# Kernel tuning notes

Measured on AMD Instinct MI355X. Metric: run time of the kernel, lower is better.

## Reference

```python
import jax, jax.numpy as jnp
import numpy as np

K = 4      # tagset_size - 2 (real emotion tags)
NT = 6     # tagset_size
START = 4
STOP = 5


def setup_inputs() -> dict:
    key = jax.random.key(0)
    ks = jax.random.split(key, 10)
    B, T = 2048, 2048
    feats = jax.random.normal(ks[0], (B, T, NT), dtype=jnp.float32)
    bias = jax.random.uniform(ks[1], (B, T), dtype=jnp.float32)        # bias_dict values in [0,1)
    tags = jax.random.randint(ks[2], (B, T), 0, K)                     # emotion labels only
    transitions = jax.random.normal(ks[3], (NT, NT), dtype=jnp.float32)
    transitions = transitions.at[START, :].set(-10000.0)
    transitions = transitions.at[:, STOP].set(-10000.0)
    w_shift_in = jax.random.normal(ks[4], (K,), dtype=jnp.float32)
    bias_no = jax.random.normal(ks[5], (1,), dtype=jnp.float32)
    bias_with = jax.random.normal(ks[6], (1,), dtype=jnp.float32)
    w_with_out = jax.random.normal(ks[7], (K,), dtype=jnp.float32)
    w_no_out = jax.random.normal(ks[8], (K,), dtype=jnp.float32)
    multiplier = jax.random.normal(ks[9], (K, K), dtype=jnp.float32)
    multiplier = multiplier.at[jnp.arange(K), jnp.arange(K)].set(-10000.0)
    return dict(feats=feats, bias=bias, tags=tags, transitions=transitions,
                w_shift_in=w_shift_in, bias_no=bias_no, bias_with=bias_with,
                w_with_out=w_with_out, w_no_out=w_no_out, multiplier=multiplier)


def reference(feats, bias, tags, transitions, w_shift_in, bias_no, bias_with,
              w_with_out, w_no_out, multiplier):
    """Batched neg_log_likelihood = forward_alg(feats) - score_sentence(feats, tags)."""
    B, T, _ = feats.shape
    # multiplier_softmax is over dim=0 (columns); diagonal overwritten with -1
    Mmod = jax.nn.softmax(multiplier, axis=0)
    Mmod = Mmod.at[jnp.arange(K), jnp.arange(K)].set(-1.0)

    # per-step transition gate, shape [B,T,K]; branch on bias > 0.5
    b = bias[..., None]
    gates = jnp.where(b > 0.5,
                      w_with_out * jnp.tanh(b * w_shift_in + bias_with),
                      w_no_out * jnp.tanh(b * w_shift_in + bias_no))

    # ---- forward algorithm (log-sum-exp DP over T, vectorized over B) ----
    init = jnp.full((B, NT), -10000.0, dtype=feats.dtype).at[:, START].set(0.0)
    feats_t = jnp.swapaxes(feats, 0, 1)   # [T,B,NT]
    gates_t = jnp.swapaxes(gates, 0, 1)   # [T,B,K]

    def step(alpha, x):
        f, g = x                                          # [B,NT], [B,K]
        blk = g[:, None, :] * Mmod[None, :, :]            # gate[prev] * Mmod[next,prev]
        Teff = transitions[None] + jnp.pad(blk, ((0, 0), (0, 2), (0, 2)))  # [B,NT,NT]
        alpha_new = f + jax.nn.logsumexp(alpha[:, None, :] + Teff, axis=2)
        return alpha_new, None

    alpha, _ = jax.lax.scan(step, init, (feats_t, gates_t))
    fwd_score = jax.nn.logsumexp(alpha + transitions[STOP][None, :], axis=1)  # [B]

    # ---- gold path score ----
    tags_ext = jnp.concatenate(
        [jnp.full((B, 1), START, dtype=tags.dtype), tags], axis=1)
    t0 = tags_ext[:, :-1]   # prev tag, [B,T]
    t1 = tags_ext[:, 1:]    # next tag, [B,T]
    base = transitions[t1, t0]
    Mext = jnp.pad(Mmod, ((0, 2), (0, 2)))
    gate_t0 = jnp.take_along_axis(gates, jnp.clip(t0, 0, K - 1)[..., None], axis=2)[..., 0]
    extra = jnp.where((t0 < K) & (t1 < K), gate_t0 * Mext[t1, t0], 0.0)
    emit = jnp.take_along_axis(feats, t1[..., None], axis=2)[..., 0]
    gold = jnp.sum(base + extra + emit, axis=1) + transitions[STOP, tags[:, -1]]

    return fwd_score - gold  # [B] per-dialog NLL
```

## Files before the change

### kernel.cpp

```cpp
#include <hip/hip_runtime.h>

#define BN 2048
#define TN 2048

__device__ __forceinline__ float ex2(float x){ return __builtin_amdgcn_exp2f(x); }
__device__ __forceinline__ float lg2(float x){ return __builtin_amdgcn_logf(x); }
__device__ __forceinline__ float rcpf(float x){ return __builtin_amdgcn_rcpf(x); }

constexpr float kLog2e = 1.4426950408889634f;
constexpr float kLn2   = 0.6931471805599453f;

__device__ __forceinline__ float fast_tanh(float x){
    float ax = fabsf(x);
    float e  = ex2(ax * (-2.0f * kLog2e));
    float t  = (1.0f - e) * rcpf(1.0f + e);
    return copysignf(t, x);
}

__device__ __forceinline__ float sel4(float v0, float v1, float v2, float v3, int idx){
    float r = (idx == 1) ? v1 : v0;
    r = (idx == 2) ? v2 : r;
    r = (idx == 3) ? v3 : r;
    return r;
}

struct P1Params {
    float AL[4][4], M[4][4];
    float wsv[4], wwv[4], wnv[4];
    float bwc, bnc;
    const float* sA; const float* sM;
};

__device__ __forceinline__ void step4(
    const P1Params& pp, float fi0, float fi1, float fi2, float fi3,
    float bv, int tg, bool renorm,
    float (&P)[4][4], float (&lacc)[4], float& gold, int& prev)
{
    const bool hw = bv > 0.5f;
    const float bc = hw ? pp.bwc : pp.bnc;
    float g[4], gL[4];
    #pragma unroll
    for (int j = 0; j < 4; ++j) {
        float x = fmaf(bv, pp.wsv[j], bc);
        g[j]  = (hw ? pp.wwv[j] : pp.wnv[j]) * fast_tanh(x);
        gL[j] = g[j] * kLog2e;
    }
    const float fiL[4] = { fi0 * kLog2e, fi1 * kLog2e, fi2 * kLog2e, fi3 * kLog2e };
    float nP[4][4];
    #pragma unroll
    for (int i = 0; i < 4; ++i)
        #pragma unroll
        for (int j = 0; j < 4; ++j) nP[i][j] = 0.0f;
    #pragma unroll
    for (int k = 0; k < 4; ++k) {
        float Ek[4];
        #pragma unroll
        for (int i = 0; i < 4; ++i)
            Ek[i] = ex2(fmaf(gL[k], pp.M[i][k], fiL[i] + pp.AL[i][k]));
        #pragma unroll
        for (int j = 0; j < 4; ++j) {
            const float pk = P[k][j];
            #pragma unroll
            for (int i = 0; i < 4; ++i) nP[i][j] = fmaf(Ek[i], pk, nP[i][j]);
        }
    }
    #pragma unroll
    for (int i = 0; i < 4; ++i)
        #pragma unroll
        for (int j = 0; j < 4; ++j) P[i][j] = nP[i][j];

    const int idx = tg * 4 + prev;
    gold += pp.sA[idx] + sel4(g[0], g[1], g[2], g[3], prev) * pp.sM[idx]
          + sel4(fi0, fi1, fi2, fi3, tg);
    prev = tg;

    if (renorm) {
        #pragma unroll
        for (int j = 0; j < 4; ++j) {
            float m = fmaxf(fmaxf(P[0][j], P[1][j]), fmaxf(P[2][j], P[3][j]));
            int ee = (int)((__float_as_uint(m) >> 23) & 255u) - 126;
            float sc = __uint_as_float((unsigned)(127 - ee) << 23);
            lacc[j] += (float)ee;
            #pragma unroll
            for (int i = 0; i < 4; ++i) P[i][j] *= sc;
        }
    }
}

__device__ __forceinline__ void compose4(
    const float (&Ae)[4][4], const float (&sa)[4],
    const float (&Be)[4][4], const float (&sb)[4],
    float (&Ce)[4][4], float (&sc)[4])
{
    const float maxA = fmaxf(fmaxf(sa[0], sa[1]), fmaxf(sa[2], sa[3]));
    float Ap[4][4];
    #pragma unroll
    for (int k = 0; k < 4; ++k) {
        const float wk = ex2(sa[k] - maxA);
        #pragma unroll
        for (int i = 0; i < 4; ++i) Ap[i][k] = Ae[i][k] * wk;
    }
    #pragma unroll
    for (int j = 0; j < 4; ++j) {
        float c0 = 0.f, c1 = 0.f, c2 = 0.f, c3 = 0.f;
        #pragma unroll
        for (int k = 0; k < 4; ++k) {
            const float bk = Be[k][j];
            c0 = fmaf(Ap[0][k], bk, c0);
            c1 = fmaf(Ap[1][k], bk, c1);
            c2 = fmaf(Ap[2][k], bk, c2);
            c3 = fmaf(Ap[3][k], bk, c3);
        }
        const float m = fmaxf(fmaxf(c0, c1), fmaxf(c2, c3));
        const int ee = (int)((__float_as_uint(m) >> 23) & 255u) - 126;
        const float scf = __uint_as_float((unsigned)(127 - ee) << 23);
        Ce[0][j] = c0 * scf; Ce[1][j] = c1 * scf;
        Ce[2][j] = c2 * scf; Ce[3][j] = c3 * scf;
        sc[j] = sb[j] + maxA + (float)ee;
    }
}

__global__ void __launch_bounds__(256)
crf_fused(const float* __restrict__ feats, const float* __restrict__ bias,
          const int* __restrict__ tags, const float* __restrict__ trans,
          const float* __restrict__ wsh, const float* __restrict__ bno,
          const float* __restrict__ bwi, const float* __restrict__ wwo,
          const float* __restrict__ wno, const float* __restrict__ mult,
          float* __restrict__ out)
{
    const int w = threadIdx.x >> 6;
    const int L = threadIdx.x & 63;
    const int b = blockIdx.x;
    const int c = threadIdx.x;

    __shared__ float shm[6400];
    __shared__ float sA[20], sM[16];
    float4* stageW = ((float4*)shm) + w * 384;

    if (threadIdx.x < 16) {
        const int i = threadIdx.x >> 2, j = threadIdx.x & 3;
        sA[threadIdx.x] = trans[i * 6 + j];
        const float m0 = mult[j], m1 = mult[4 + j], m2 = mult[8 + j], m3 = mult[12 + j];
        const float mx = fmaxf(fmaxf(m0, m1), fmaxf(m2, m3));
        const float e0 = ex2((m0 - mx) * kLog2e), e1 = ex2((m1 - mx) * kLog2e);
        const float e2 = ex2((m2 - mx) * kLog2e), e3 = ex2((m3 - mx) * kLog2e);
        const float inv = rcpf(e0 + e1 + e2 + e3);
        const float ei = (i == 0) ? e0 : (i == 1) ? e1 : (i == 2) ? e2 : e3;
        sM[threadIdx.x] = (i == j) ? -1.0f : ei * inv;
        if (threadIdx.x < 4) sA[16 + threadIdx.x] = trans[threadIdx.x * 6 + 4];
    }
    __syncthreads();

    P1Params pp;
    #pragma unroll
    for (int i = 0; i < 4; ++i)
        #pragma unroll
        for (int j = 0; j < 4; ++j) {
            pp.AL[i][j] = trans[i * 6 + j] * kLog2e;
            pp.M[i][j]  = sM[i * 4 + j];
        }
    #pragma unroll
    for (int j = 0; j < 4; ++j) { pp.wsv[j] = wsh[j]; pp.wwv[j] = wwo[j]; pp.wnv[j] = wno[j]; }
    pp.bwc = bwi[0]; pp.bnc = bno[0];
    pp.sA = sA; pp.sM = sM;

    int prev = 0;
    if (c != 0) prev = tags[(size_t)b * TN + c * 8 - 1];

    const float4* gF = (const float4*)feats + (size_t)b * 3072 + (size_t)w * 768;

    float P[4][4], lacc[4] = {0.f, 0.f, 0.f, 0.f};
    #pragma unroll
    for (int i = 0; i < 4; ++i)
        #pragma unroll
        for (int j = 0; j < 4; ++j) P[i][j] = (i == j) ? 1.0f : 0.0f;
    float gold = 0.0f;
    const bool isC0 = (c == 0);

    #pragma unroll 1
    for (int h = 0; h < 2; ++h) {
        float4 myF[6];
        {
            float4 tF[6];
            const int h6 = h * 6;
            #pragma unroll
            for (int r = 0; r < 6; ++r) {
                const int S  = r * 64 + L;
                const int cS = (S * 10923) >> 16;
                const int j  = S - cS * 6;
                tF[r] = gF[cS * 12 + h6 + j];
            }
            #pragma unroll
            for (int r = 0; r < 6; ++r) {
                const int S  = r * 64 + L;
                const int cS = (S * 10923) >> 16;
                const int j  = S - cS * 6;
                stageW[(j << 6) + ((cS + j) & 63)] = tF[r];
            }
            #pragma unroll
            for (int j = 0; j < 6; ++j)
                myF[j] = stageW[(j << 6) + ((L + j) & 63)];
        }
        float Bv[4]; int Tg[4];
        {
            const float4 b4 = *(const float4*)(bias + (size_t)b * TN + c * 8 + h * 4);
            Bv[0]=b4.x; Bv[1]=b4.y; Bv[2]=b4.z; Bv[3]=b4.w;
            const int4 t4 = *(const int4*)(tags + (size_t)b * TN + c * 8 + h * 4);
            Tg[0]=t4.x; Tg[1]=t4.y; Tg[2]=t4.z; Tg[3]=t4.w;
        }
        const bool init0 = isC0 && (h == 0);
        #pragma unroll
        for (int p = 0; p < 2; ++p) {
            const float4 fA = myF[3*p], fB = myF[3*p+1], fC = myF[3*p+2];
            {
                const float fi0 = fA.x, fi1 = fA.y, fi2 = fA.z, fi3 = fA.w;
                if (init0 && p == 0) {
                    const float a0 = fi0 + sA[16], a1 = fi1 + sA[17];
                    const float a2 = fi2 + sA[18], a3 = fi3 + sA[19];
                    const float mx = fmaxf(fmaxf(a0, a1), fmaxf(a2, a3));
                    const float e0 = ex2((a0 - mx) * kLog2e);
                    const float e1 = ex2((a1 - mx) * kLog2e);
                    const float e2 = ex2((a2 - mx) * kLog2e);
                    const float e3 = ex2((a3 - mx) * kLog2e);
                    #pragma unroll
                    for (int j = 0; j < 4; ++j) {
                        P[0][j] = e0; P[1][j] = e1; P[2][j] = e2; P[3][j] = e3;
                        lacc[j] = mx * kLog2e;
                    }
                    const int tg0 = Tg[0];
                    gold = sel4(sA[16], sA[17], sA[18], sA[19], tg0)
                         + sel4(fi0, fi1, fi2, fi3, tg0);
                    prev = tg0;
                } else {
                    step4(pp, fi0, fi1, fi2, fi3, Bv[2*p], Tg[2*p],
                          false, P, lacc, gold, prev);
                }
            }
            {
                const float fi0 = fB.z, fi1 = fB.w, fi2 = fC.x, fi3 = fC.y;
                step4(pp, fi0, fi1, fi2, fi3, Bv[2*p+1], Tg[2*p+1],
                      (2*p+1) == 3, P, lacc, gold, prev);
            }
        }
    }

    __syncthreads();
    {
        float* my = shm + (size_t)c * 25;
        #pragma unroll
        for (int i = 0; i < 4; ++i)
            #pragma unroll
            for (int j = 0; j < 4; ++j) my[i * 4 + j] = P[i][j];
        #pragma unroll
        for (int j = 0; j < 4; ++j) my[16 + j] = lacc[j];
        my[20] = gold;
    }
    #pragma unroll 1
    for (int l = 0; l < 8; ++l) {
        __syncthreads();
        const int cnt = 128 >> l;
        if (threadIdx.x < cnt) {
            float* se = shm + (size_t)(threadIdx.x << (l + 1)) * 25;
            const float* sl = se + (25 << l);
            float Be_[4][4], sb[4], Ae[4][4], sa[4];
            #pragma unroll
            for (int i = 0; i < 4; ++i)
                #pragma unroll
                for (int j = 0; j < 4; ++j) { Be_[i][j] = se[i*4+j]; Ae[i][j] = sl[i*4+j]; }
            #pragma unroll
            for (int j = 0; j < 4; ++j) { sb[j] = se[16+j]; sa[j] = sl[16+j]; }
            const float gsum = se[20] + sl[20];
            float Ce[4][4], sc[4];
            compose4(Ae, sa, Be_, sb, Ce, sc);
            #pragma unroll
            for (int i = 0; i < 4; ++i)
                #pragma unroll
                for (int j = 0; j < 4; ++j) se[i*4+j] = Ce[i][j];
            #pragma unroll
            for (int j = 0; j < 4; ++j) se[16+j] = sc[j];
            se[20] = gsum;
        }
    }

    if (threadIdx.x == 0) {
        const float p00 = shm[0], p10 = shm[4], p20 = shm[8], p30 = shm[12];
        const float so0 = shm[16];
        const float gall = shm[20];
        const float t50 = trans[30], t51 = trans[31], t52 = trans[32], t53 = trans[33];
        const float ssum = p00 * ex2(t50 * kLog2e) + p10 * ex2(t51 * kLog2e)
                         + p20 * ex2(t52 * kLog2e) + p30 * ex2(t53 * kLog2e);
        const float fwd = (so0 + lg2(ssum)) * kLn2;
        const int lastT = tags[(size_t)b * TN + TN - 1];
        const float gfin = gall + sel4(t50, t51, t52, t53, lastT);
        out[b] = fwd - gfin;
    }
}

extern "C" void kernel_launch(void* const* d_in, const int* in_sizes, int n_in,
                              void* d_out, int out_size, void* d_ws, size_t ws_size,
                              hipStream_t stream)
{
    const float* feats = (const float*)d_in[0];
    const float* bias  = (const float*)d_in[1];
    const int*   tags  = (const int*)d_in[2];
    const float* trans = (const float*)d_in[3];
    const float* wsh   = (const float*)d_in[4];
    const float* bno   = (const float*)d_in[5];
    const float* bwi   = (const float*)d_in[6];
    const float* wwo   = (const float*)d_in[7];
    const float* wno   = (const float*)d_in[8];
    const float* mult  = (const float*)d_in[9];
    float* out = (float*)d_out;
    (void)d_ws; (void)ws_size;

    crf_fused<<<BN, 256, 0, stream>>>(
        feats, bias, tags, trans, wsh, bno, bwi, wwo, wno, mult, out);
}
```

Before: 209.7 us.

## Prefetch second half of feats while processing first, scalarize uniform params

The per-half loop is fully unrolled, and the global loads for the second half of feats, bias and tags are issued before the first half is processed, so their latency overlaps compute. Uniform parameters (transitions, softmaxed multiplier, gate weights, start transitions) are passed through readfirstlane so the compiler can keep them in scalar registers, freeing vector registers. The staging reads are moved into the step loop instead of being held in a register array. Prefetching and full unrolling raise register pressure, which could reduce occupancy.

Result: faster. 197.2 us (-6.0%).

```diff
diff --git a/kernel.cpp b/kernel.cpp
--- a/kernel.cpp
+++ b/kernel.cpp
@@ -6,6 +6,9 @@
 __device__ __forceinline__ float ex2(float x){ return __builtin_amdgcn_exp2f(x); }
 __device__ __forceinline__ float lg2(float x){ return __builtin_amdgcn_logf(x); }
 __device__ __forceinline__ float rcpf(float x){ return __builtin_amdgcn_rcpf(x); }
+__device__ __forceinline__ float rfl(float x){
+    return __uint_as_float(__builtin_amdgcn_readfirstlane(__float_as_uint(x)));
+}
 
 constexpr float kLog2e = 1.4426950408889634f;
 constexpr float kLn2   = 0.6931471805599453f;
@@ -156,18 +159,29 @@
     for (int i = 0; i < 4; ++i)
         #pragma unroll
         for (int j = 0; j < 4; ++j) {
-            pp.AL[i][j] = trans[i * 6 + j] * kLog2e;
-            pp.M[i][j]  = sM[i * 4 + j];
-        }
-    #pragma unroll
-    for (int j = 0; j < 4; ++j) { pp.wsv[j] = wsh[j]; pp.wwv[j] = wwo[j]; pp.wnv[j] = wno[j]; }
-    pp.bwc = bwi[0]; pp.bnc = bno[0];
+            pp.AL[i][j] = rfl(trans[i * 6 + j] * kLog2e);
+            pp.M[i][j]  = rfl(sM[i * 4 + j]);
+        }
+    #pragma unroll
+    for (int j = 0; j < 4; ++j) {
+        pp.wsv[j] = rfl(wsh[j]); pp.wwv[j] = rfl(wwo[j]); pp.wnv[j] = rfl(wno[j]);
+    }
+    pp.bwc = rfl(bwi[0]); pp.bnc = rfl(bno[0]);
     pp.sA = sA; pp.sM = sM;
+    const float tcI0 = rfl(sA[16]), tcI1 = rfl(sA[17]);
+    const float tcI2 = rfl(sA[18]), tcI3 = rfl(sA[19]);
 
     int prev = 0;
     if (c != 0) prev = tags[(size_t)b * TN + c * 8 - 1];
 
     const float4* gF = (const float4*)feats + (size_t)b * 3072 + (size_t)w * 768;
+
+    int offI[6];
+    #pragma unroll
+    for (int r = 0; r < 6; ++r) {
+        const int S = r * 64 + L, cS = (S * 10923) >> 16;
+        offI[r] = cS * 12 + (S - cS * 6);
+    }
 
     float P[4][4], lacc[4] = {0.f, 0.f, 0.f, 0.f};
     #pragma unroll
@@ -177,46 +191,38 @@
     float gold = 0.0f;
     const bool isC0 = (c == 0);
 
-    #pragma unroll 1
+    float4 tF[6];
+    #pragma unroll
+    for (int r = 0; r < 6; ++r) tF[r] = gF[offI[r]];
+    float4 bv4 = *(const float4*)(bias + (size_t)b * TN + c * 8);
+    int4   tg4 = *(const int4*)(tags + (size_t)b * TN + c * 8);
+
+    #pragma unroll
     for (int h = 0; h < 2; ++h) {
-        float4 myF[6];
-        {
-            float4 tF[6];
-            const int h6 = h * 6;
-            #pragma unroll
-            for (int r = 0; r < 6; ++r) {
-                const int S  = r * 64 + L;
-                const int cS = (S * 10923) >> 16;
-                const int j  = S - cS * 6;
-                tF[r] = gF[cS * 12 + h6 + j];
-            }
-            #pragma unroll
-            for (int r = 0; r < 6; ++r) {
-                const int S  = r * 64 + L;
-                const int cS = (S * 10923) >> 16;
-                const int j  = S - cS * 6;
-                stageW[(j << 6) + ((cS + j) & 63)] = tF[r];
-            }
-            #pragma unroll
-            for (int j = 0; j < 6; ++j)
-                myF[j] = stageW[(j << 6) + ((L + j) & 63)];
-        }
-        float Bv[4]; int Tg[4];
-        {
-            const float4 b4 = *(const float4*)(bias + (size_t)b * TN + c * 8 + h * 4);
-            Bv[0]=b4.x; Bv[1]=b4.y; Bv[2]=b4.z; Bv[3]=b4.w;
-            const int4 t4 = *(const int4*)(tags + (size_t)b * TN + c * 8 + h * 4);
-            Tg[0]=t4.x; Tg[1]=t4.y; Tg[2]=t4.z; Tg[3]=t4.w;
+        #pragma unroll
+        for (int r = 0; r < 6; ++r) {
+            const int S = r * 64 + L, cS = (S * 10923) >> 16, j = S - cS * 6;
+            stageW[(j << 6) + ((cS + j) & 63)] = tF[r];
+        }
+        const float Bv[4] = { bv4.x, bv4.y, bv4.z, bv4.w };
+        const int   Tg[4] = { tg4.x, tg4.y, tg4.z, tg4.w };
+        if (h == 0) {
+            #pragma unroll
+            for (int r = 0; r < 6; ++r) tF[r] = gF[offI[r] + 6];
+            bv4 = *(const float4*)(bias + (size_t)b * TN + c * 8 + 4);
+            tg4 = *(const int4*)(tags + (size_t)b * TN + c * 8 + 4);
         }
         const bool init0 = isC0 && (h == 0);
         #pragma unroll
         for (int p = 0; p < 2; ++p) {
-            const float4 fA = myF[3*p], fB = myF[3*p+1], fC = myF[3*p+2];
+            const float4 fA = stageW[((3*p+0) << 6) + ((L + 3*p+0) & 63)];
+            const float4 fB = stageW[((3*p+1) << 6) + ((L + 3*p+1) & 63)];
+            const float4 fC = stageW[((3*p+2) << 6) + ((L + 3*p+2) & 63)];
             {
                 const float fi0 = fA.x, fi1 = fA.y, fi2 = fA.z, fi3 = fA.w;
                 if (init0 && p == 0) {
-                    const float a0 = fi0 + sA[16], a1 = fi1 + sA[17];
-                    const float a2 = fi2 + sA[18], a3 = fi3 + sA[19];
+                    const float a0 = fi0 + tcI0, a1 = fi1 + tcI1;
+                    const float a2 = fi2 + tcI2, a3 = fi3 + tcI3;
                     const float mx = fmaxf(fmaxf(a0, a1), fmaxf(a2, a3));
                     const float e0 = ex2((a0 - mx) * kLog2e);
                     const float e1 = ex2((a1 - mx) * kLog2e);
@@ -228,7 +234,7 @@
                         lacc[j] = mx * kLog2e;
                     }
                     const int tg0 = Tg[0];
-                    gold = sel4(sA[16], sA[17], sA[18], sA[19], tg0)
+                    gold = sel4(tcI0, tcI1, tcI2, tcI3, tg0)
                          + sel4(fi0, fi1, fi2, fi3, tg0);
                     prev = tg0;
                 } else {
```
